# Kernel tuning notes

Hardware: AMD Instinct MI355X
Metric: run time of the kernel (lower is better)

Reference implementation:

```python
import jax, jax.numpy as jnp
import numpy as np

N_NODES = 50000
N_EDGES = 800000
D = 128


def gcn_conv(x, W, b, src, dst, num_nodes):
    """PyG GCNConv: x @ W, add self-loops, symmetric normalization, scatter-add, + bias."""
    x = x @ W  # [N, out]
    loop = jnp.arange(num_nodes, dtype=src.dtype)
    s = jnp.concatenate([src, loop])  # [E+N]
    d = jnp.concatenate([dst, loop])
    w = jnp.ones(s.shape[0], x.dtype)  # edge_weight=None -> ones (self-loop fill=1)
    deg = jax.ops.segment_sum(w, d, num_segments=num_nodes)  # [N]
    dinv = jnp.where(deg > 0, jax.lax.rsqrt(deg), 0.0)
    norm = dinv[s] * dinv[d]  # [E+N]
    out = jax.ops.segment_sum(x[s] * norm[:, None], d, num_segments=num_nodes)
    return out + b


def setup_inputs() -> dict:
    key = jax.random.key(0)
    ks = jax.random.split(key, 8)
    sc = 1.0 / np.sqrt(D)
    x = jax.random.normal(ks[0], (N_NODES, D), dtype=jnp.float32)
    edge_index = jax.random.randint(ks[1], (2, N_EDGES), 0, N_NODES)
    W1 = jax.random.normal(ks[2], (D, D), dtype=jnp.float32) * sc
    W2 = jax.random.normal(ks[3], (D, D), dtype=jnp.float32) * sc
    W3 = jax.random.normal(ks[4], (D, D), dtype=jnp.float32) * sc
    b1 = jnp.zeros((D,), jnp.float32)
    b2 = jnp.zeros((D,), jnp.float32)
    b3 = jnp.zeros((D,), jnp.float32)
    return {"x": x, "edge_index": edge_index, "W1": W1, "b1": b1,
            "W2": W2, "b2": b2, "W3": W3, "b3": b3}


def reference(x, edge_index, W1, b1, W2, b2, W3, b3):
    src, dst = edge_index[0], edge_index[1]
    n = x.shape[0]
    x = jax.nn.relu(gcn_conv(x, W1, b1, src, dst, n))
    x = jax.nn.relu(gcn_conv(x, W2, b2, src, dst, n))
    return gcn_conv(x, W3, b3, src, dst, n)
```

## Files before the change

### kernel.cpp

```cpp
#include <hip/hip_runtime.h>
#include <hip/hip_fp16.h>
#include <math.h>

#define D 128
#define PADH 136

typedef __attribute__((ext_vector_type(8))) _Float16 half8;
typedef __attribute__((ext_vector_type(4))) float f32x4;


__global__ void prep_kernel(const float* __restrict__ W1, const float* __restrict__ W2,
                            const float* __restrict__ W3, __half* __restrict__ WhT,
                            int* __restrict__ cnt, int N) {
    int i = blockIdx.x * blockDim.x + threadIdx.x;
    if (i < 3 * D * D) {
        int l = i >> 14;
        int j = i & 16383;
        int n = j >> 7, k = j & 127;
        const float* W = (l == 0) ? W1 : (l == 1) ? W2 : W3;
        WhT[(size_t)i] = __float2half(W[(size_t)k * D + n]);
    }
    if (i < N) cnt[i] = 0;
}


__global__ void count_rank_kernel(const int* __restrict__ dst, int* __restrict__ cnt,
                                  int* __restrict__ rank, int E) {
    int e0 = (blockIdx.x * blockDim.x + threadIdx.x) * 8;
    if (e0 + 7 < E) {
        int4 da = *(const int4*)(dst + e0);
        int4 db = *(const int4*)(dst + e0 + 4);
        int4 ra, rb;
        ra.x = atomicAdd(&cnt[da.x], 1);
        ra.y = atomicAdd(&cnt[da.y], 1);
        ra.z = atomicAdd(&cnt[da.z], 1);
        ra.w = atomicAdd(&cnt[da.w], 1);
        rb.x = atomicAdd(&cnt[db.x], 1);
        rb.y = atomicAdd(&cnt[db.y], 1);
        rb.z = atomicAdd(&cnt[db.z], 1);
        rb.w = atomicAdd(&cnt[db.w], 1);
        *(int4*)(rank + e0)     = ra;
        *(int4*)(rank + e0 + 4) = rb;
    } else {
        for (int e = e0; e < E; ++e) rank[e] = atomicAdd(&cnt[dst[e]], 1);
    }
}

__global__ __launch_bounds__(1024) void scan_kernel(const int* __restrict__ cnt,
                                                    int* __restrict__ rowptr,
                                                    float* __restrict__ dinv,
                                                    int N) {
    __shared__ int wsum[16];
    int tid  = threadIdx.x;
    int lane = tid & 63;
    int wid  = tid >> 6;
    int C = ((N + 4095) / 4096) * 4;
    int start = tid * C;
    int end   = start + C; if (end > N) end = N;

    int local = 0;
    int i = start;
    for (; i + 3 < end; i += 4) {
        int4 v = *(const int4*)(cnt + i);
        local += v.x + v.y + v.z + v.w;
    }
    for (; i < end; ++i) local += cnt[i];

    int sc = local;
    #pragma unroll
    for (int off = 1; off < 64; off <<= 1) {
        int t = __shfl_up(sc, off, 64);
        if (lane >= off) sc += t;
    }
    if (lane == 63) wsum[wid] = sc;
    __syncthreads();
    if (tid < 16) {
        int w = wsum[tid];
        #pragma unroll
        for (int off = 1; off < 16; off <<= 1) {
            int t = __shfl_up(w, off, 16);
            if (tid >= off) w += t;
        }
        wsum[tid] = w;
    }
    __syncthreads();
    int run = ((wid > 0) ? wsum[wid - 1] : 0) + (sc - local);

    i = start;
    for (; i + 3 < end; i += 4) {
        int4 v = *(const int4*)(cnt + i);
        int4 rp;
        rp.x = run;
        rp.y = rp.x + v.x;
        rp.z = rp.y + v.y;
        rp.w = rp.z + v.z;
        run  = rp.w + v.w;
        *(int4*)(rowptr + i) = rp;
        float4 dv;
        dv.x = rsqrtf((float)v.x + 1.0f);
        dv.y = rsqrtf((float)v.y + 1.0f);
        dv.z = rsqrtf((float)v.z + 1.0f);
        dv.w = rsqrtf((float)v.w + 1.0f);
        *(float4*)(dinv + i) = dv;
    }
    for (; i < end; ++i) {
        int v = cnt[i];
        rowptr[i] = run; run += v;
        dinv[i] = rsqrtf((float)v + 1.0f);
    }
    if (tid == 0) rowptr[N] = wsum[15];
}


#define GATHER(vv, cc) __half2 vv = ((const __half2*)(g + (size_t)(cc) * D))[lane]

__device__ __forceinline__ float2 gather_row(const __half* __restrict__ g,
                                             const int* __restrict__ rowptr,
                                             const int* __restrict__ col,
                                             int row, int lane) {
    int s = rowptr[row], e = rowptr[row + 1];
    __half2 hself = ((const __half2*)(g + (size_t)row * D))[lane];
    float2 a0 = __half22float2(hself);
    float2 a1 = make_float2(0.f, 0.f), a2 = make_float2(0.f, 0.f),
           a3 = make_float2(0.f, 0.f), a4 = make_float2(0.f, 0.f),
           a5 = make_float2(0.f, 0.f), a6 = make_float2(0.f, 0.f),
           a7 = make_float2(0.f, 0.f);

    for (int base = s; base < e; base += 64) {
        int idx = base + lane;
        int myc = (idx < e) ? col[idx] : 0;
        int nb  = min(64, e - base);
        int j = 0;
        for (; j + 16 <= nb; j += 16) {
            int c0 = __shfl(myc, j + 0),  c1 = __shfl(myc, j + 1);
            int c2 = __shfl(myc, j + 2),  c3 = __shfl(myc, j + 3);
            int c4 = __shfl(myc, j + 4),  c5 = __shfl(myc, j + 5);
            int c6 = __shfl(myc, j + 6),  c7 = __shfl(myc, j + 7);
            int c8 = __shfl(myc, j + 8),  c9 = __shfl(myc, j + 9);
            int cA = __shfl(myc, j + 10), cB = __shfl(myc, j + 11);
            int cC = __shfl(myc, j + 12), cD = __shfl(myc, j + 13);
            int cE = __shfl(myc, j + 14), cF = __shfl(myc, j + 15);
            GATHER(v0, c0); GATHER(v1, c1); GATHER(v2, c2); GATHER(v3, c3);
            GATHER(v4, c4); GATHER(v5, c5); GATHER(v6, c6); GATHER(v7, c7);
            GATHER(v8, c8); GATHER(v9, c9); GATHER(vA, cA); GATHER(vB, cB);
            GATHER(vC, cC); GATHER(vD, cD); GATHER(vE, cE); GATHER(vF, cF);
            a0.x += __low2float(v0); a0.y += __high2float(v0);
            a1.x += __low2float(v1); a1.y += __high2float(v1);
            a2.x += __low2float(v2); a2.y += __high2float(v2);
            a3.x += __low2float(v3); a3.y += __high2float(v3);
            a4.x += __low2float(v4); a4.y += __high2float(v4);
            a5.x += __low2float(v5); a5.y += __high2float(v5);
            a6.x += __low2float(v6); a6.y += __high2float(v6);
            a7.x += __low2float(v7); a7.y += __high2float(v7);
            a0.x += __low2float(v8); a0.y += __high2float(v8);
            a1.x += __low2float(v9); a1.y += __high2float(v9);
            a2.x += __low2float(vA); a2.y += __high2float(vA);
            a3.x += __low2float(vB); a3.y += __high2float(vB);
            a4.x += __low2float(vC); a4.y += __high2float(vC);
            a5.x += __low2float(vD); a5.y += __high2float(vD);
            a6.x += __low2float(vE); a6.y += __high2float(vE);
            a7.x += __low2float(vF); a7.y += __high2float(vF);
        }
        for (; j + 8 <= nb; j += 8) {
            int c0 = __shfl(myc, j + 0), c1 = __shfl(myc, j + 1);
            int c2 = __shfl(myc, j + 2), c3 = __shfl(myc, j + 3);
            int c4 = __shfl(myc, j + 4), c5 = __shfl(myc, j + 5);
            int c6 = __shfl(myc, j + 6), c7 = __shfl(myc, j + 7);
            GATHER(v0, c0); GATHER(v1, c1); GATHER(v2, c2); GATHER(v3, c3);
            GATHER(v4, c4); GATHER(v5, c5); GATHER(v6, c6); GATHER(v7, c7);
            a0.x += __low2float(v0); a0.y += __high2float(v0);
            a1.x += __low2float(v1); a1.y += __high2float(v1);
            a2.x += __low2float(v2); a2.y += __high2float(v2);
            a3.x += __low2float(v3); a3.y += __high2float(v3);
            a4.x += __low2float(v4); a4.y += __high2float(v4);
            a5.x += __low2float(v5); a5.y += __high2float(v5);
            a6.x += __low2float(v6); a6.y += __high2float(v6);
            a7.x += __low2float(v7); a7.y += __high2float(v7);
        }
        for (; j + 4 <= nb; j += 4) {
            int c0 = __shfl(myc, j + 0), c1 = __shfl(myc, j + 1);
            int c2 = __shfl(myc, j + 2), c3 = __shfl(myc, j + 3);
            GATHER(v0, c0); GATHER(v1, c1); GATHER(v2, c2); GATHER(v3, c3);
            a0.x += __low2float(v0); a0.y += __high2float(v0);
            a1.x += __low2float(v1); a1.y += __high2float(v1);
            a2.x += __low2float(v2); a2.y += __high2float(v2);
            a3.x += __low2float(v3); a3.y += __high2float(v3);
        }
        for (; j < nb; ++j) {
            int c = __shfl(myc, j);
            GATHER(v, c);
            a0.x += __low2float(v); a0.y += __high2float(v);
        }
    }
    a0.x += a1.x + a2.x + a3.x + a4.x + a5.x + a6.x + a7.x;
    a0.y += a1.y + a2.y + a3.y + a4.y + a5.y + a6.y + a7.y;
    return a0;
}


__global__ __launch_bounds__(256) void fill_gemm1_kernel(
    const int* __restrict__ src, const int* __restrict__ dst,
    const int* __restrict__ rank, const int* __restrict__ rowptr,
    int* __restrict__ col, int E, int fill_blocks,
    const float* __restrict__ X, const __half* __restrict__ WhT,
    const float* __restrict__ dinv, __half* __restrict__ Y, int M) {
    int tid = threadIdx.x;
    if ((int)blockIdx.x < fill_blocks) {
        int e0 = (blockIdx.x * 256 + tid) * 8;
        if (e0 + 7 < E) {
            int4 da = *(const int4*)(dst + e0);
            int4 db = *(const int4*)(dst + e0 + 4);
            int4 ra = *(const int4*)(rank + e0);
            int4 rb = *(const int4*)(rank + e0 + 4);
            int4 sa = *(const int4*)(src + e0);
            int4 sb = *(const int4*)(src + e0 + 4);
            int p0 = rowptr[da.x] + ra.x;
            int p1 = rowptr[da.y] + ra.y;
            int p2 = rowptr[da.z] + ra.z;
            int p3 = rowptr[da.w] + ra.w;
            int p4 = rowptr[db.x] + rb.x;
            int p5 = rowptr[db.y] + rb.y;
            int p6 = rowptr[db.z] + rb.z;
            int p7 = rowptr[db.w] + rb.w;
            col[p0] = sa.x; col[p1] = sa.y; col[p2] = sa.z; col[p3] = sa.w;
            col[p4] = sb.x; col[p5] = sb.y; col[p6] = sb.z; col[p7] = sb.w;
        } else {
            for (int e = e0; e < E; ++e) col[rowptr[dst[e]] + rank[e]] = src[e];
        }
        return;
    }
    int bid  = blockIdx.x - fill_blocks;
    int wave = tid >> 6;
    int lane = tid & 63;
    int quad = lane >> 4;
    int l16  = lane & 15;
    int m0   = bid * 64 + wave * 16;
    if (m0 >= M) return;

    f32x4 acc[8];
    #pragma unroll
    for (int t = 0; t < 8; ++t) acc[t] = (f32x4)0.0f;

    const float* xrow = X + (size_t)(m0 + l16) * D;

    #pragma unroll
    for (int ks = 0; ks < 4; ++ks) {
        int k0 = ks * 32 + quad * 8;
        float4 x0 = *(const float4*)(xrow + k0);
        float4 x1 = *(const float4*)(xrow + k0 + 4);
        half8 a;
        a[0] = (_Float16)x0.x; a[1] = (_Float16)x0.y;
        a[2] = (_Float16)x0.z; a[3] = (_Float16)x0.w;
        a[4] = (_Float16)x1.x; a[5] = (_Float16)x1.y;
        a[6] = (_Float16)x1.z; a[7] = (_Float16)x1.w;
        #pragma unroll
        for (int t = 0; t < 8; ++t) {
            half8 b = *(const half8*)(WhT + (size_t)(t * 16 + l16) * D + k0);
            acc[t] = __builtin_amdgcn_mfma_f32_16x16x32_f16(a, b, acc[t], 0, 0, 0);
        }
    }

    float4 dv = *(const float4*)(dinv + m0 + quad * 4);
    float dvs[4] = {dv.x, dv.y, dv.z, dv.w};
    #pragma unroll
    for (int t = 0; t < 8; ++t) {
        #pragma unroll
        for (int r = 0; r < 4; ++r) {
            int grow = m0 + quad * 4 + r;
            Y[(size_t)grow * D + t * 16 + l16] = __float2half(acc[t][r] * dvs[r]);
        }
    }
}


__global__ __launch_bounds__(256) void agg_gemm_kernel(
    const __half* __restrict__ ysIn, const int* __restrict__ rowptr,
    const int* __restrict__ col, const float* __restrict__ dinv,
    const float* __restrict__ bias, const __half* __restrict__ WhT,
    __half* __restrict__ ysOut, int M) {
    __shared__ __half lds_h[16 * PADH];
    int tid  = threadIdx.x;
    int wave = tid >> 6;
    int lane = tid & 63;
    int rbase = blockIdx.x * 16;

    float2 bb = ((const float2*)bias)[lane];
    #pragma unroll
    for (int t = 0; t < 4; ++t) {
        int row = rbase + wave * 4 + t;
        if (row < M) {
            float2 a = gather_row(ysIn, rowptr, col, row, lane);
            float dv = dinv[row];
            float rx = bb.x + dv * a.x;
            float ry = bb.y + dv * a.y;
            __half2 hv = __floats2half2_rn(fmaxf(rx, 0.f), fmaxf(ry, 0.f));
            ((__half2*)(lds_h + (size_t)(wave * 4 + t) * PADH))[lane] = hv;
        }
    }
    __syncthreads();

    if (rbase >= M) return;
    int quad = lane >> 4;
    int l16  = lane & 15;
    int t0   = wave * 2;

    f32x4 acc0 = (f32x4)0.0f, acc1 = (f32x4)0.0f;
    const __half* arow = lds_h + (size_t)l16 * PADH;

    #pragma unroll
    for (int ks = 0; ks < 4; ++ks) {
        int k0 = ks * 32 + quad * 8;
        half8 a  = *(const half8*)(arow + k0);
        half8 b0 = *(const half8*)(WhT + (size_t)((t0 + 0) * 16 + l16) * D + k0);
        half8 b1 = *(const half8*)(WhT + (size_t)((t0 + 1) * 16 + l16) * D + k0);
        acc0 = __builtin_amdgcn_mfma_f32_16x16x32_f16(a, b0, acc0, 0, 0, 0);
        acc1 = __builtin_amdgcn_mfma_f32_16x16x32_f16(a, b1, acc1, 0, 0, 0);
    }

    #pragma unroll
    for (int r = 0; r < 4; ++r) {
        int grow = rbase + quad * 4 + r;
        if (grow < M) {
            float dvr = dinv[grow];
            ysOut[(size_t)grow * D + (t0 + 0) * 16 + l16] = __float2half(acc0[r] * dvr);
            ysOut[(size_t)grow * D + (t0 + 1) * 16 + l16] = __float2half(acc1[r] * dvr);
        }
    }
}


__global__ __launch_bounds__(256) void agg_final_kernel(
    const __half* __restrict__ ys, const int* __restrict__ rowptr,
    const int* __restrict__ col, const float* __restrict__ dinv,
    const float* __restrict__ b, float* __restrict__ out, int N) {
    int gwave = (blockIdx.x * blockDim.x + threadIdx.x) >> 6;
    int lane  = threadIdx.x & 63;
    if (gwave >= N) return;
    float2 a  = gather_row(ys, rowptr, col, gwave, lane);
    float dv  = dinv[gwave];
    float2 bb = ((const float2*)b)[lane];
    ((float2*)(out + (size_t)gwave * D))[lane] = make_float2(bb.x + dv * a.x, bb.y + dv * a.y);
}


extern "C" void kernel_launch(void* const* d_in, const int* in_sizes, int n_in,
                              void* d_out, int out_size, void* d_ws, size_t ws_size,
                              hipStream_t stream) {
    const float* x   = (const float*)d_in[0];
    const int*   ei  = (const int*)d_in[1];
    const float* W1  = (const float*)d_in[2];
    const float* b1  = (const float*)d_in[3];
    const float* W2  = (const float*)d_in[4];
    const float* b2  = (const float*)d_in[5];
    const float* W3  = (const float*)d_in[6];
    const float* b3  = (const float*)d_in[7];
    float* out = (float*)d_out;

    const int N = in_sizes[0] / D;
    const int E = in_sizes[1] / 2;
    const int* src = ei;
    const int* dst = ei + E;

    char* ws = (char*)d_ws;
    size_t off = 0;
    auto alloc = [&](size_t bytes) {
        void* p = ws + off;
        off = (off + bytes + 255) & ~(size_t)255;
        return p;
    };
    __half* ys    = (__half*)alloc((size_t)N * D * sizeof(__half));
    __half* hs    = (__half*)alloc((size_t)N * D * sizeof(__half));
    int*   cnt    = (int*)alloc((size_t)N * sizeof(int));
    int*   rowptr = (int*)alloc((size_t)(N + 1) * sizeof(int));
    float* dinv   = (float*)alloc((size_t)N * sizeof(float));
    int*   rank   = (int*)alloc((size_t)E * sizeof(int));
    int*   col    = (int*)alloc((size_t)E * sizeof(int));
    __half* WhT   = (__half*)alloc((size_t)3 * D * D * sizeof(__half));
    (void)ws_size; (void)n_in; (void)out_size;

    int prep_threads = (3 * D * D > N) ? 3 * D * D : N;
    prep_kernel<<<(prep_threads + 255) / 256, 256, 0, stream>>>(W1, W2, W3, WhT, cnt, N);

    const int egrid = ((E + 7) / 8 + 255) / 256;
    count_rank_kernel<<<egrid, 256, 0, stream>>>(dst, cnt, rank, E);
    scan_kernel<<<1, 1024, 0, stream>>>(cnt, rowptr, dinv, N);

    const int gemm1_grid = (N + 63) / 64;
    fill_gemm1_kernel<<<egrid + gemm1_grid, 256, 0, stream>>>(
        src, dst, rank, rowptr, col, E, egrid, x, WhT, dinv, ys, N);

    const int agg_gemm_grid = (N + 15) / 16;
    agg_gemm_kernel<<<agg_gemm_grid, 256, 0, stream>>>(ys, rowptr, col, dinv, b1, WhT + 16384, hs, N);
    agg_gemm_kernel<<<agg_gemm_grid, 256, 0, stream>>>(hs, rowptr, col, dinv, b2, WhT + 32768, ys, N);

    const int agg_grid = (N * 64 + 255) / 256;
    agg_final_kernel<<<agg_grid, 256, 0, stream>>>(ys, rowptr, col, dinv, b3, out, N);
}
```

Before: 311.4 us.

## Build CSR with atomic cursors and use 8-wave blocks for agg_gemm

```diff
diff --git a/kernel.cpp b/kernel.cpp
--- a/kernel.cpp
+++ b/kernel.cpp
@@ -24,30 +24,27 @@
 }
 
 
-__global__ void count_rank_kernel(const int* __restrict__ dst, int* __restrict__ cnt,
-                                  int* __restrict__ rank, int E) {
+__global__ void count_kernel(const int* __restrict__ dst, int* __restrict__ cnt, int E) {
     int e0 = (blockIdx.x * blockDim.x + threadIdx.x) * 8;
     if (e0 + 7 < E) {
         int4 da = *(const int4*)(dst + e0);
         int4 db = *(const int4*)(dst + e0 + 4);
-        int4 ra, rb;
-        ra.x = atomicAdd(&cnt[da.x], 1);
-        ra.y = atomicAdd(&cnt[da.y], 1);
-        ra.z = atomicAdd(&cnt[da.z], 1);
-        ra.w = atomicAdd(&cnt[da.w], 1);
-        rb.x = atomicAdd(&cnt[db.x], 1);
-        rb.y = atomicAdd(&cnt[db.y], 1);
-        rb.z = atomicAdd(&cnt[db.z], 1);
-        rb.w = atomicAdd(&cnt[db.w], 1);
-        *(int4*)(rank + e0)     = ra;
-        *(int4*)(rank + e0 + 4) = rb;
+        atomicAdd(&cnt[da.x], 1);
+        atomicAdd(&cnt[da.y], 1);
+        atomicAdd(&cnt[da.z], 1);
+        atomicAdd(&cnt[da.w], 1);
+        atomicAdd(&cnt[db.x], 1);
+        atomicAdd(&cnt[db.y], 1);
+        atomicAdd(&cnt[db.z], 1);
+        atomicAdd(&cnt[db.w], 1);
     } else {
-        for (int e = e0; e < E; ++e) rank[e] = atomicAdd(&cnt[dst[e]], 1);
+        for (int e = e0; e < E; ++e) atomicAdd(&cnt[dst[e]], 1);
     }
 }
 
 __global__ __launch_bounds__(1024) void scan_kernel(const int* __restrict__ cnt,
                                                     int* __restrict__ rowptr,
+                                                    int* __restrict__ cursor,
                                                     float* __restrict__ dinv,
                                                     int N) {
     __shared__ int wsum[16];
@@ -96,6 +93,7 @@
         rp.w = rp.z + v.z;
         run  = rp.w + v.w;
         *(int4*)(rowptr + i) = rp;
+        *(int4*)(cursor + i) = rp;
         float4 dv;
         dv.x = rsqrtf((float)v.x + 1.0f);
         dv.y = rsqrtf((float)v.y + 1.0f);
@@ -105,7 +103,7 @@
     }
     for (; i < end; ++i) {
         int v = cnt[i];
-        rowptr[i] = run; run += v;
+        rowptr[i] = run; cursor[i] = run; run += v;
         dinv[i] = rsqrtf((float)v + 1.0f);
     }
     if (tid == 0) rowptr[N] = wsum[15];
@@ -200,8 +198,7 @@
 
 __global__ __launch_bounds__(256) void fill_gemm1_kernel(
     const int* __restrict__ src, const int* __restrict__ dst,
-    const int* __restrict__ rank, const int* __restrict__ rowptr,
-    int* __restrict__ col, int E, int fill_blocks,
+    int* __restrict__ cursor, int* __restrict__ col, int E, int fill_blocks,
     const float* __restrict__ X, const __half* __restrict__ WhT,
     const float* __restrict__ dinv, __half* __restrict__ Y, int M) {
     int tid = threadIdx.x;
@@ -210,22 +207,23 @@
         if (e0 + 7 < E) {
             int4 da = *(const int4*)(dst + e0);
             int4 db = *(const int4*)(dst + e0 + 4);
-            int4 ra = *(const int4*)(rank + e0);
-            int4 rb = *(const int4*)(rank + e0 + 4);
             int4 sa = *(const int4*)(src + e0);
             int4 sb = *(const int4*)(src + e0 + 4);
-            int p0 = rowptr[da.x] + ra.x;
-            int p1 = rowptr[da.y] + ra.y;
-            int p2 = rowptr[da.z] + ra.z;
-            int p3 = rowptr[da.w] + ra.w;
-            int p4 = rowptr[db.x] + rb.x;
-            int p5 = rowptr[db.y] + rb.y;
-            int p6 = rowptr[db.z] + rb.z;
-            int p7 = rowptr[db.w] + rb.w;
+            int p0 = atomicAdd(&cursor[da.x], 1);
+            int p1 = atomicAdd(&cursor[da.y], 1);
+            int p2 = atomicAdd(&cursor[da.z], 1);
+            int p3 = atomicAdd(&cursor[da.w], 1);
+            int p4 = atomicAdd(&cursor[db.x], 1);
+            int p5 = atomicAdd(&cursor[db.y], 1);
+            int p6 = atomicAdd(&cursor[db.z], 1);
+            int p7 = atomicAdd(&cursor[db.w], 1);
             col[p0] = sa.x; col[p1] = sa.y; col[p2] = sa.z; col[p3] = sa.w;
             col[p4] = sb.x; col[p5] = sb.y; col[p6] = sb.z; col[p7] = sb.w;
         } else {
-            for (int e = e0; e < E; ++e) col[rowptr[dst[e]] + rank[e]] = src[e];
+            for (int e = e0; e < E; ++e) {
+                int p = atomicAdd(&cursor[dst[e]], 1);
+                col[p] = src[e];
+            }
         }
         return;
     }
@@ -273,7 +271,7 @@
 }
 
 
-__global__ __launch_bounds__(256) void agg_gemm_kernel(
+__global__ __launch_bounds__(512) void agg_gemm_kernel(
     const __half* __restrict__ ysIn, const int* __restrict__ rowptr,
     const int* __restrict__ col, const float* __restrict__ dinv,
     const float* __restrict__ bias, const __half* __restrict__ WhT,
@@ -286,15 +284,16 @@
 
     float2 bb = ((const float2*)bias)[lane];
     #pragma unroll
-    for (int t = 0; t < 4; ++t) {
-        int row = rbase + wave * 4 + t;
+    for (int t = 0; t < 2; ++t) {
+        int r   = wave * 2 + t;
+        int row = rbase + r;
         if (row < M) {
             float2 a = gather_row(ysIn, rowptr, col, row, lane);
             float dv = dinv[row];
             float rx = bb.x + dv * a.x;
             float ry = bb.y + dv * a.y;
             __half2 hv = __floats2half2_rn(fmaxf(rx, 0.f), fmaxf(ry, 0.f));
-            ((__half2*)(lds_h + (size_t)(wave * 4 + t) * PADH))[lane] = hv;
+            ((__half2*)(lds_h + (size_t)r * PADH))[lane] = hv;
         }
     }
     __syncthreads();
@@ -302,19 +301,16 @@
     if (rbase >= M) return;
     int quad = lane >> 4;
     int l16  = lane & 15;
-    int t0   = wave * 2;
-
-    f32x4 acc0 = (f32x4)0.0f, acc1 = (f32x4)0.0f;
+
+    f32x4 acc = (f32x4)0.0f;
     const __half* arow = lds_h + (size_t)l16 * PADH;
 
     #pragma unroll
     for (int ks = 0; ks < 4; ++ks) {
         int k0 = ks * 32 + quad * 8;
-        half8 a  = *(const half8*)(arow + k0);
-        half8 b0 = *(const half8*)(WhT + (size_t)((t0 + 0) * 16 + l16) * D + k0);
-        half8 b1 = *(const half8*)(WhT + (size_t)((t0 + 1) * 16 + l16) * D + k0);
-        acc0 = __builtin_amdgcn_mfma_f32_16x16x32_f16(a, b0, acc0, 0, 0, 0);
-        acc1 = __builtin_amdgcn_mfma_f32_16x16x32_f16(a, b1, acc1, 0, 0, 0);
+        half8 a = *(const half8*)(arow + k0);
+        half8 b = *(const half8*)(WhT + (size_t)(wave * 16 + l16) * D + k0);
+        acc = __builtin_amdgcn_mfma_f32_16x16x32_f16(a, b, acc, 0, 0, 0);
     }
 
     #pragma unroll
@@ -322,8 +318,7 @@
         int grow = rbase + quad * 4 + r;
         if (grow < M) {
             float dvr = dinv[grow];
-            ysOut[(size_t)grow * D + (t0 + 0) * 16 + l16] = __float2half(acc0[r] * dvr);
-            ysOut[(size_t)grow * D + (t0 + 1) * 16 + l16] = __float2half(acc1[r] * dvr);
+            ysOut[(size_t)grow * D + wave * 16 + l16] = __float2half(acc[r] * dvr);
         }
     }
 }
@@ -372,8 +367,8 @@
     __half* hs    = (__half*)alloc((size_t)N * D * sizeof(__half));
     int*   cnt    = (int*)alloc((size_t)N * sizeof(int));
     int*   rowptr = (int*)alloc((size_t)(N + 1) * sizeof(int));
+    int*   cursor = (int*)alloc((size_t)N * sizeof(int));
     float* dinv   = (float*)alloc((size_t)N * sizeof(float));
-    int*   rank   = (int*)alloc((size_t)E * sizeof(int));
     int*   col    = (int*)alloc((size_t)E * sizeof(int));
     __half* WhT   = (__half*)alloc((size_t)3 * D * D * sizeof(__half));
     (void)ws_size; (void)n_in; (void)out_size;
@@ -382,16 +377,16 @@
     prep_kernel<<<(prep_threads + 255) / 256, 256, 0, stream>>>(W1, W2, W3, WhT, cnt, N);
 
     const int egrid = ((E + 7) / 8 + 255) / 256;
-    count_rank_kernel<<<egrid, 256, 0, stream>>>(dst, cnt, rank, E);
-    scan_kernel<<<1, 1024, 0, stream>>>(cnt, rowptr, dinv, N);
+    count_kernel<<<egrid, 256, 0, stream>>>(dst, cnt, E);
+    scan_kernel<<<1, 1024, 0, stream>>>(cnt, rowptr, cursor, dinv, N);
 
     const int gemm1_grid = (N + 63) / 64;
     fill_gemm1_kernel<<<egrid + gemm1_grid, 256, 0, stream>>>(
-        src, dst, rank, rowptr, col, E, egrid, x, WhT, dinv, ys, N);
+        src, dst, cursor, col, E, egrid, x, WhT, dinv, ys, N);
 
     const int agg_gemm_grid = (N + 15) / 16;
-    agg_gemm_kernel<<<agg_gemm_grid, 256, 0, stream>>>(ys, rowptr, col, dinv, b1, WhT + 16384, hs, N);
-    agg_gemm_kernel<<<agg_gemm_grid, 256, 0, stream>>>(hs, rowptr, col, dinv, b2, WhT + 32768, ys, N);
+    agg_gemm_kernel<<<agg_gemm_grid, 512, 0, stream>>>(ys, rowptr, col, dinv, b1, WhT + 16384, hs, N);
+    agg_gemm_kernel<<<agg_gemm_grid, 512, 0, stream>>>(hs, rowptr, col, dinv, b2, WhT + 32768, ys, N);
 
     const int agg_grid = (N * 64 + 255) / 256;
     agg_final_kernel<<<agg_grid, 256, 0, stream>>>(ys, rowptr, col, dinv, b3, out, N);
```

After: 340.5 us. +9.3%, slower.

## Split each wave into two half-waves gathering separate rows with 8-byte loads

Applied to the files above, without the earlier changes.

```diff
diff --git a/kernel.cpp b/kernel.cpp
--- a/kernel.cpp
+++ b/kernel.cpp
@@ -6,6 +6,7 @@
 #define PADH 136
 
 typedef __attribute__((ext_vector_type(8))) _Float16 half8;
+typedef __attribute__((ext_vector_type(4))) _Float16 half4v;
 typedef __attribute__((ext_vector_type(4))) float f32x4;
 
 
@@ -112,89 +113,67 @@
 }
 
 
-#define GATHER(vv, cc) __half2 vv = ((const __half2*)(g + (size_t)(cc) * D))[lane]
-
-__device__ __forceinline__ float2 gather_row(const __half* __restrict__ g,
-                                             const int* __restrict__ rowptr,
-                                             const int* __restrict__ col,
-                                             int row, int lane) {
+__device__ __forceinline__ float4 gather2(const __half* __restrict__ g,
+                                          const int* __restrict__ rowptr,
+                                          const int* __restrict__ col,
+                                          int r0, int r1, int lane) {
+    int half = lane >> 5;
+    int l32  = lane & 31;
+    int hb   = half << 5;
+    int row  = half ? r1 : r0;
     int s = rowptr[row], e = rowptr[row + 1];
-    __half2 hself = ((const __half2*)(g + (size_t)row * D))[lane];
-    float2 a0 = __half22float2(hself);
-    float2 a1 = make_float2(0.f, 0.f), a2 = make_float2(0.f, 0.f),
-           a3 = make_float2(0.f, 0.f), a4 = make_float2(0.f, 0.f),
-           a5 = make_float2(0.f, 0.f), a6 = make_float2(0.f, 0.f),
-           a7 = make_float2(0.f, 0.f);
-
-    for (int base = s; base < e; base += 64) {
-        int idx = base + lane;
+
+    half4v hs = ((const half4v*)(g + (size_t)row * D))[l32];
+    float4 A = make_float4((float)hs[0], (float)hs[1], (float)hs[2], (float)hs[3]);
+    float4 B = make_float4(0.f, 0.f, 0.f, 0.f);
+
+    for (int base = s; base < e; base += 32) {
+        int idx = base + l32;
         int myc = (idx < e) ? col[idx] : 0;
-        int nb  = min(64, e - base);
+        int nb  = min(32, e - base);
         int j = 0;
-        for (; j + 16 <= nb; j += 16) {
-            int c0 = __shfl(myc, j + 0),  c1 = __shfl(myc, j + 1);
-            int c2 = __shfl(myc, j + 2),  c3 = __shfl(myc, j + 3);
-            int c4 = __shfl(myc, j + 4),  c5 = __shfl(myc, j + 5);
-            int c6 = __shfl(myc, j + 6),  c7 = __shfl(myc, j + 7);
-            int c8 = __shfl(myc, j + 8),  c9 = __shfl(myc, j + 9);
-            int cA = __shfl(myc, j + 10), cB = __shfl(myc, j + 11);
-            int cC = __shfl(myc, j + 12), cD = __shfl(myc, j + 13);
-            int cE = __shfl(myc, j + 14), cF = __shfl(myc, j + 15);
-            GATHER(v0, c0); GATHER(v1, c1); GATHER(v2, c2); GATHER(v3, c3);
-            GATHER(v4, c4); GATHER(v5, c5); GATHER(v6, c6); GATHER(v7, c7);
-            GATHER(v8, c8); GATHER(v9, c9); GATHER(vA, cA); GATHER(vB, cB);
-            GATHER(vC, cC); GATHER(vD, cD); GATHER(vE, cE); GATHER(vF, cF);
-            a0.x += __low2float(v0); a0.y += __high2float(v0);
-            a1.x += __low2float(v1); a1.y += __high2float(v1);
-            a2.x += __low2float(v2); a2.y += __high2float(v2);
-            a3.x += __low2float(v3); a3.y += __high2float(v3);
-            a4.x += __low2float(v4); a4.y += __high2float(v4);
-            a5.x += __low2float(v5); a5.y += __high2float(v5);
-            a6.x += __low2float(v6); a6.y += __high2float(v6);
-            a7.x += __low2float(v7); a7.y += __high2float(v7);
-            a0.x += __low2float(v8); a0.y += __high2float(v8);
-            a1.x += __low2float(v9); a1.y += __high2float(v9);
-            a2.x += __low2float(vA); a2.y += __high2float(vA);
-            a3.x += __low2float(vB); a3.y += __high2float(vB);
-            a4.x += __low2float(vC); a4.y += __high2float(vC);
-            a5.x += __low2float(vD); a5.y += __high2float(vD);
-            a6.x += __low2float(vE); a6.y += __high2float(vE);
-            a7.x += __low2float(vF); a7.y += __high2float(vF);
-        }
         for (; j + 8 <= nb; j += 8) {
-            int c0 = __shfl(myc, j + 0), c1 = __shfl(myc, j + 1);
-            int c2 = __shfl(myc, j + 2), c3 = __shfl(myc, j + 3);
-            int c4 = __shfl(myc, j + 4), c5 = __shfl(myc, j + 5);
-            int c6 = __shfl(myc, j + 6), c7 = __shfl(myc, j + 7);
-            GATHER(v0, c0); GATHER(v1, c1); GATHER(v2, c2); GATHER(v3, c3);
-            GATHER(v4, c4); GATHER(v5, c5); GATHER(v6, c6); GATHER(v7, c7);
-            a0.x += __low2float(v0); a0.y += __high2float(v0);
-            a1.x += __low2float(v1); a1.y += __high2float(v1);
-            a2.x += __low2float(v2); a2.y += __high2float(v2);
-            a3.x += __low2float(v3); a3.y += __high2float(v3);
-            a4.x += __low2float(v4); a4.y += __high2float(v4);
-            a5.x += __low2float(v5); a5.y += __high2float(v5);
-            a6.x += __low2float(v6); a6.y += __high2float(v6);
-            a7.x += __low2float(v7); a7.y += __high2float(v7);
+            int c0 = __shfl(myc, hb + j + 0), c1 = __shfl(myc, hb + j + 1);
+            int c2 = __shfl(myc, hb + j + 2), c3 = __shfl(myc, hb + j + 3);
+            int c4 = __shfl(myc, hb + j + 4), c5 = __shfl(myc, hb + j + 5);
+            int c6 = __shfl(myc, hb + j + 6), c7 = __shfl(myc, hb + j + 7);
+            half4v v0 = ((const half4v*)(g + (size_t)c0 * D))[l32];
+            half4v v1 = ((const half4v*)(g + (size_t)c1 * D))[l32];
+            half4v v2 = ((const half4v*)(g + (size_t)c2 * D))[l32];
+            half4v v3 = ((const half4v*)(g + (size_t)c3 * D))[l32];
+            half4v v4 = ((const half4v*)(g + (size_t)c4 * D))[l32];
+            half4v v5 = ((const half4v*)(g + (size_t)c5 * D))[l32];
+            half4v v6 = ((const half4v*)(g + (size_t)c6 * D))[l32];
+            half4v v7 = ((const half4v*)(g + (size_t)c7 * D))[l32];
+            A.x += (float)v0[0]; A.y += (float)v0[1]; A.z += (float)v0[2]; A.w += (float)v0[3];
+            B.x += (float)v1[0]; B.y += (float)v1[1]; B.z += (float)v1[2]; B.w += (float)v1[3];
+            A.x += (float)v2[0]; A.y += (float)v2[1]; A.z += (float)v2[2]; A.w += (float)v2[3];
+            B.x += (float)v3[0]; B.y += (float)v3[1]; B.z += (float)v3[2]; B.w += (float)v3[3];
+            A.x += (float)v4[0]; A.y += (float)v4[1]; A.z += (float)v4[2]; A.w += (float)v4[3];
+            B.x += (float)v5[0]; B.y += (float)v5[1]; B.z += (float)v5[2]; B.w += (float)v5[3];
+            A.x += (float)v6[0]; A.y += (float)v6[1]; A.z += (float)v6[2]; A.w += (float)v6[3];
+            B.x += (float)v7[0]; B.y += (float)v7[1]; B.z += (float)v7[2]; B.w += (float)v7[3];
         }
         for (; j + 4 <= nb; j += 4) {
-            int c0 = __shfl(myc, j + 0), c1 = __shfl(myc, j + 1);
-            int c2 = __shfl(myc, j + 2), c3 = __shfl(myc, j + 3);
-            GATHER(v0, c0); GATHER(v1, c1); GATHER(v2, c2); GATHER(v3, c3);
-            a0.x += __low2float(v0); a0.y += __high2float(v0);
-            a1.x += __low2float(v1); a1.y += __high2float(v1);
-            a2.x += __low2float(v2); a2.y += __high2float(v2);
-            a3.x += __low2float(v3); a3.y += __high2float(v3);
+            int c0 = __shfl(myc, hb + j + 0), c1 = __shfl(myc, hb + j + 1);
+            int c2 = __shfl(myc, hb + j + 2), c3 = __shfl(myc, hb + j + 3);
+            half4v v0 = ((const half4v*)(g + (size_t)c0 * D))[l32];
+            half4v v1 = ((const half4v*)(g + (size_t)c1 * D))[l32];
+            half4v v2 = ((const half4v*)(g + (size_t)c2 * D))[l32];
+            half4v v3 = ((const half4v*)(g + (size_t)c3 * D))[l32];
+            A.x += (float)v0[0]; A.y += (float)v0[1]; A.z += (float)v0[2]; A.w += (float)v0[3];
+            B.x += (float)v1[0]; B.y += (float)v1[1]; B.z += (float)v1[2]; B.w += (float)v1[3];
+            A.x += (float)v2[0]; A.y += (float)v2[1]; A.z += (float)v2[2]; A.w += (float)v2[3];
+            B.x += (float)v3[0]; B.y += (float)v3[1]; B.z += (float)v3[2]; B.w += (float)v3[3];
         }
         for (; j < nb; ++j) {
-            int c = __shfl(myc, j);
-            GATHER(v, c);
-            a0.x += __low2float(v); a0.y += __high2float(v);
-        }
-    }
-    a0.x += a1.x + a2.x + a3.x + a4.x + a5.x + a6.x + a7.x;
-    a0.y += a1.y + a2.y + a3.y + a4.y + a5.y + a6.y + a7.y;
-    return a0;
+            int c = __shfl(myc, hb + j);
+            half4v v = ((const half4v*)(g + (size_t)c * D))[l32];
+            A.x += (float)v[0]; A.y += (float)v[1]; A.z += (float)v[2]; A.w += (float)v[3];
+        }
+    }
+    A.x += B.x; A.y += B.y; A.z += B.z; A.w += B.w;
+    return A;
 }
 
 
@@ -282,20 +261,27 @@
     int tid  = threadIdx.x;
     int wave = tid >> 6;
     int lane = tid & 63;
+    int half = lane >> 5;
+    int l32  = lane & 31;
     int rbase = blockIdx.x * 16;
 
-    float2 bb = ((const float2*)bias)[lane];
-    #pragma unroll
-    for (int t = 0; t < 4; ++t) {
-        int row = rbase + wave * 4 + t;
-        if (row < M) {
-            float2 a = gather_row(ysIn, rowptr, col, row, lane);
-            float dv = dinv[row];
-            float rx = bb.x + dv * a.x;
-            float ry = bb.y + dv * a.y;
-            __half2 hv = __floats2half2_rn(fmaxf(rx, 0.f), fmaxf(ry, 0.f));
-            ((__half2*)(lds_h + (size_t)(wave * 4 + t) * PADH))[lane] = hv;
-        }
+    float4 bb = ((const float4*)bias)[l32];
+    #pragma unroll
+    for (int t = 0; t < 2; ++t) {
+        int lr0 = wave * 4 + t * 2;
+        int row0 = rbase + lr0;
+        int row1 = row0 + 1;
+        int c0 = min(row0, M - 1);
+        int c1 = min(row1, M - 1);
+        float4 a = gather2(ysIn, rowptr, col, c0, c1, lane);
+        int myrow = half ? c1 : c0;
+        float dv = dinv[myrow];
+        half4v hv;
+        hv[0] = (_Float16)fmaxf(bb.x + dv * a.x, 0.f);
+        hv[1] = (_Float16)fmaxf(bb.y + dv * a.y, 0.f);
+        hv[2] = (_Float16)fmaxf(bb.z + dv * a.z, 0.f);
+        hv[3] = (_Float16)fmaxf(bb.w + dv * a.w, 0.f);
+        ((half4v*)(lds_h + (size_t)(lr0 + half) * PADH))[l32] = hv;
     }
     __syncthreads();
 
@@ -335,11 +321,26 @@
     const float* __restrict__ b, float* __restrict__ out, int N) {
     int gwave = (blockIdx.x * blockDim.x + threadIdx.x) >> 6;
     int lane  = threadIdx.x & 63;
-    if (gwave >= N) return;
-    float2 a  = gather_row(ys, rowptr, col, gwave, lane);
-    float dv  = dinv[gwave];
-    float2 bb = ((const float2*)b)[lane];
-    ((float2*)(out + (size_t)gwave * D))[lane] = make_float2(bb.x + dv * a.x, bb.y + dv * a.y);
+    int half  = lane >> 5;
+    int l32   = lane & 31;
+    int row0  = gwave * 2;
+    if (row0 >= N) return;
+    int row1  = row0 + 1;
+    int c1    = min(row1, N - 1);
+
+    float4 a = gather2(ys, rowptr, col, row0, c1, lane);
+    int myrow = half ? c1 : row0;
+    int orow  = row0 + half;
+    if (orow < N) {
+        float dv  = dinv[myrow];
+        float4 bb = ((const float4*)b)[l32];
+        float4 r;
+        r.x = bb.x + dv * a.x;
+        r.y = bb.y + dv * a.y;
+        r.z = bb.z + dv * a.z;
+        r.w = bb.w + dv * a.w;
+        ((float4*)(out + (size_t)orow * D))[l32] = r;
+    }
 }
 
 
@@ -393,6 +394,6 @@
     agg_gemm_kernel<<<agg_gemm_grid, 256, 0, stream>>>(ys, rowptr, col, dinv, b1, WhT + 16384, hs, N);
     agg_gemm_kernel<<<agg_gemm_grid, 256, 0, stream>>>(hs, rowptr, col, dinv, b2, WhT + 32768, ys, N);
 
-    const int agg_grid = (N * 64 + 255) / 256;
-    agg_final_kernel<<<agg_grid, 256, 0, stream>>>(ys, rowptr, col, dinv, b3, out, N);
-}
+    const int aggf_grid = ((N + 1) / 2 * 64 + 255) / 256;
+    agg_final_kernel<<<aggf_grid, 256, 0, stream>>>(ys, rowptr, col, dinv, b3, out, N);
+}
```

Result: faster. 294.2 us (-5.5%).

## Slice features into 16-wide column blocks so gathers stay cache-resident

Applied to the files above, without the earlier changes.

```diff
diff --git a/kernel.cpp b/kernel.cpp
--- a/kernel.cpp
+++ b/kernel.cpp
@@ -3,10 +3,10 @@
 #include <math.h>
 
 #define D 128
-#define PADH 136
 
 typedef __attribute__((ext_vector_type(8))) _Float16 half8;
 typedef __attribute__((ext_vector_type(4))) float f32x4;
+
 
 
 __global__ void prep_kernel(const float* __restrict__ W1, const float* __restrict__ W2,
@@ -109,92 +109,6 @@
         dinv[i] = rsqrtf((float)v + 1.0f);
     }
     if (tid == 0) rowptr[N] = wsum[15];
-}
-
-
-#define GATHER(vv, cc) __half2 vv = ((const __half2*)(g + (size_t)(cc) * D))[lane]
-
-__device__ __forceinline__ float2 gather_row(const __half* __restrict__ g,
-                                             const int* __restrict__ rowptr,
-                                             const int* __restrict__ col,
-                                             int row, int lane) {
-    int s = rowptr[row], e = rowptr[row + 1];
-    __half2 hself = ((const __half2*)(g + (size_t)row * D))[lane];
-    float2 a0 = __half22float2(hself);
-    float2 a1 = make_float2(0.f, 0.f), a2 = make_float2(0.f, 0.f),
-           a3 = make_float2(0.f, 0.f), a4 = make_float2(0.f, 0.f),
-           a5 = make_float2(0.f, 0.f), a6 = make_float2(0.f, 0.f),
-           a7 = make_float2(0.f, 0.f);
-
-    for (int base = s; base < e; base += 64) {
-        int idx = base + lane;
-        int myc = (idx < e) ? col[idx] : 0;
-        int nb  = min(64, e - base);
-        int j = 0;
-        for (; j + 16 <= nb; j += 16) {
-            int c0 = __shfl(myc, j + 0),  c1 = __shfl(myc, j + 1);
-            int c2 = __shfl(myc, j + 2),  c3 = __shfl(myc, j + 3);
-            int c4 = __shfl(myc, j + 4),  c5 = __shfl(myc, j + 5);
-            int c6 = __shfl(myc, j + 6),  c7 = __shfl(myc, j + 7);
-            int c8 = __shfl(myc, j + 8),  c9 = __shfl(myc, j + 9);
-            int cA = __shfl(myc, j + 10), cB = __shfl(myc, j + 11);
-            int cC = __shfl(myc, j + 12), cD = __shfl(myc, j + 13);
-            int cE = __shfl(myc, j + 14), cF = __shfl(myc, j + 15);
-            GATHER(v0, c0); GATHER(v1, c1); GATHER(v2, c2); GATHER(v3, c3);
-            GATHER(v4, c4); GATHER(v5, c5); GATHER(v6, c6); GATHER(v7, c7);
-            GATHER(v8, c8); GATHER(v9, c9); GATHER(vA, cA); GATHER(vB, cB);
-            GATHER(vC, cC); GATHER(vD, cD); GATHER(vE, cE); GATHER(vF, cF);
-            a0.x += __low2float(v0); a0.y += __high2float(v0);
-            a1.x += __low2float(v1); a1.y += __high2float(v1);
-            a2.x += __low2float(v2); a2.y += __high2float(v2);
-            a3.x += __low2float(v3); a3.y += __high2float(v3);
-            a4.x += __low2float(v4); a4.y += __high2float(v4);
-            a5.x += __low2float(v5); a5.y += __high2float(v5);
-            a6.x += __low2float(v6); a6.y += __high2float(v6);
-            a7.x += __low2float(v7); a7.y += __high2float(v7);
-            a0.x += __low2float(v8); a0.y += __high2float(v8);
-            a1.x += __low2float(v9); a1.y += __high2float(v9);
-            a2.x += __low2float(vA); a2.y += __high2float(vA);
-            a3.x += __low2float(vB); a3.y += __high2float(vB);
-            a4.x += __low2float(vC); a4.y += __high2float(vC);
-            a5.x += __low2float(vD); a5.y += __high2float(vD);
-            a6.x += __low2float(vE); a6.y += __high2float(vE);
-            a7.x += __low2float(vF); a7.y += __high2float(vF);
-        }
-        for (; j + 8 <= nb; j += 8) {
-            int c0 = __shfl(myc, j + 0), c1 = __shfl(myc, j + 1);
-            int c2 = __shfl(myc, j + 2), c3 = __shfl(myc, j + 3);
-            int c4 = __shfl(myc, j + 4), c5 = __shfl(myc, j + 5);
-            int c6 = __shfl(myc, j + 6), c7 = __shfl(myc, j + 7);
-            GATHER(v0, c0); GATHER(v1, c1); GATHER(v2, c2); GATHER(v3, c3);
-            GATHER(v4, c4); GATHER(v5, c5); GATHER(v6, c6); GATHER(v7, c7);
-            a0.x += __low2float(v0); a0.y += __high2float(v0);
-            a1.x += __low2float(v1); a1.y += __high2float(v1);
-            a2.x += __low2float(v2); a2.y += __high2float(v2);
-            a3.x += __low2float(v3); a3.y += __high2float(v3);
-            a4.x += __low2float(v4); a4.y += __high2float(v4);
-            a5.x += __low2float(v5); a5.y += __high2float(v5);
-            a6.x += __low2float(v6); a6.y += __high2float(v6);
-            a7.x += __low2float(v7); a7.y += __high2float(v7);
-        }
-        for (; j + 4 <= nb; j += 4) {
-            int c0 = __shfl(myc, j + 0), c1 = __shfl(myc, j + 1);
-            int c2 = __shfl(myc, j + 2), c3 = __shfl(myc, j + 3);
-            GATHER(v0, c0); GATHER(v1, c1); GATHER(v2, c2); GATHER(v3, c3);
-            a0.x += __low2float(v0); a0.y += __high2float(v0);
-            a1.x += __low2float(v1); a1.y += __high2float(v1);
-            a2.x += __low2float(v2); a2.y += __high2float(v2);
-            a3.x += __low2float(v3); a3.y += __high2float(v3);
-        }
-        for (; j < nb; ++j) {
-            int c = __shfl(myc, j);
-            GATHER(v, c);
-            a0.x += __low2float(v); a0.y += __high2float(v);
-        }
-    }
-    a0.x += a1.x + a2.x + a3.x + a4.x + a5.x + a6.x + a7.x;
-    a0.y += a1.y + a2.y + a3.y + a4.y + a5.y + a6.y + a7.y;
-    return a0;
 }
 
 
@@ -267,79 +181,132 @@
         #pragma unroll
         for (int r = 0; r < 4; ++r) {
             int grow = m0 + quad * 4 + r;
-            Y[(size_t)grow * D + t * 16 + l16] = __float2half(acc[t][r] * dvs[r]);
-        }
-    }
-}
-
-
-__global__ __launch_bounds__(256) void agg_gemm_kernel(
-    const __half* __restrict__ ysIn, const int* __restrict__ rowptr,
-    const int* __restrict__ col, const float* __restrict__ dinv,
-    const float* __restrict__ bias, const __half* __restrict__ WhT,
-    __half* __restrict__ ysOut, int M) {
-    __shared__ __half lds_h[16 * PADH];
+            Y[((size_t)t * M + grow) * 16 + l16] = __float2half(acc[t][r] * dvs[r]);
+        }
+    }
+}
+
+
+__global__ __launch_bounds__(256) void gemm_s_kernel(const __half* __restrict__ Xs,
+                                                     const __half* __restrict__ WhT,
+                                                     const float* __restrict__ dinv,
+                                                     __half* __restrict__ Ys, int M) {
     int tid  = threadIdx.x;
     int wave = tid >> 6;
     int lane = tid & 63;
-    int rbase = blockIdx.x * 16;
-
-    float2 bb = ((const float2*)bias)[lane];
-    #pragma unroll
-    for (int t = 0; t < 4; ++t) {
-        int row = rbase + wave * 4 + t;
-        if (row < M) {
-            float2 a = gather_row(ysIn, rowptr, col, row, lane);
-            float dv = dinv[row];
-            float rx = bb.x + dv * a.x;
-            float ry = bb.y + dv * a.y;
-            __half2 hv = __floats2half2_rn(fmaxf(rx, 0.f), fmaxf(ry, 0.f));
-            ((__half2*)(lds_h + (size_t)(wave * 4 + t) * PADH))[lane] = hv;
-        }
-    }
-    __syncthreads();
-
-    if (rbase >= M) return;
     int quad = lane >> 4;
     int l16  = lane & 15;
-    int t0   = wave * 2;
-
-    f32x4 acc0 = (f32x4)0.0f, acc1 = (f32x4)0.0f;
-    const __half* arow = lds_h + (size_t)l16 * PADH;
+    int m0   = blockIdx.x * 64 + wave * 16;
+    if (m0 >= M) return;
+
+    f32x4 acc[8];
+    #pragma unroll
+    for (int t = 0; t < 8; ++t) acc[t] = (f32x4)0.0f;
+
+    int arow = m0 + l16;
 
     #pragma unroll
     for (int ks = 0; ks < 4; ++ks) {
         int k0 = ks * 32 + quad * 8;
-        half8 a  = *(const half8*)(arow + k0);
-        half8 b0 = *(const half8*)(WhT + (size_t)((t0 + 0) * 16 + l16) * D + k0);
-        half8 b1 = *(const half8*)(WhT + (size_t)((t0 + 1) * 16 + l16) * D + k0);
-        acc0 = __builtin_amdgcn_mfma_f32_16x16x32_f16(a, b0, acc0, 0, 0, 0);
-        acc1 = __builtin_amdgcn_mfma_f32_16x16x32_f16(a, b1, acc1, 0, 0, 0);
-    }
-
-    #pragma unroll
-    for (int r = 0; r < 4; ++r) {
-        int grow = rbase + quad * 4 + r;
-        if (grow < M) {
-            float dvr = dinv[grow];
-            ysOut[(size_t)grow * D + (t0 + 0) * 16 + l16] = __float2half(acc0[r] * dvr);
-            ysOut[(size_t)grow * D + (t0 + 1) * 16 + l16] = __float2half(acc1[r] * dvr);
-        }
-    }
-}
-
-
-__global__ __launch_bounds__(256) void agg_final_kernel(
-    const __half* __restrict__ ys, const int* __restrict__ rowptr,
+        half8 a = *(const half8*)(Xs + ((size_t)(k0 >> 4) * M + arow) * 16 + (k0 & 15));
+        #pragma unroll
+        for (int t = 0; t < 8; ++t) {
+            half8 b = *(const half8*)(WhT + (size_t)(t * 16 + l16) * D + k0);
+            acc[t] = __builtin_amdgcn_mfma_f32_16x16x32_f16(a, b, acc[t], 0, 0, 0);
+        }
+    }
+
+    float4 dv = *(const float4*)(dinv + m0 + quad * 4);
+    float dvs[4] = {dv.x, dv.y, dv.z, dv.w};
+    #pragma unroll
+    for (int t = 0; t < 8; ++t) {
+        #pragma unroll
+        for (int r = 0; r < 4; ++r) {
+            int grow = m0 + quad * 4 + r;
+            Ys[((size_t)t * M + grow) * 16 + l16] = __float2half(acc[t][r] * dvs[r]);
+        }
+    }
+}
+
+
+template <bool FINAL>
+__global__ __launch_bounds__(256) void agg_slice_kernel(
+    const __half* __restrict__ ysIn, const int* __restrict__ rowptr,
     const int* __restrict__ col, const float* __restrict__ dinv,
-    const float* __restrict__ b, float* __restrict__ out, int N) {
-    int gwave = (blockIdx.x * blockDim.x + threadIdx.x) >> 6;
-    int lane  = threadIdx.x & 63;
-    if (gwave >= N) return;
-    float2 a  = gather_row(ys, rowptr, col, gwave, lane);
-    float dv  = dinv[gwave];
-    float2 bb = ((const float2*)b)[lane];
-    ((float2*)(out + (size_t)gwave * D))[lane] = make_float2(bb.x + dv * a.x, bb.y + dv * a.y);
+    const float* __restrict__ bias, __half* __restrict__ outh,
+    float* __restrict__ outf, int M) {
+    int bid   = blockIdx.x;
+    int slice = bid & 7;
+    int chunk = bid >> 3;
+    int tid  = threadIdx.x;
+    int wave = tid >> 6;
+    int lane = tid & 63;
+    int g    = lane >> 3;
+    int l8   = lane & 7;
+    int row  = chunk * 32 + wave * 8 + g;
+    bool valid = row < M;
+    int c = valid ? row : M - 1;
+
+    const __half* base = ysIn + (size_t)slice * M * 16;
+    int s = rowptr[c], e = rowptr[c + 1];
+
+    float2 bb = ((const float2*)bias)[slice * 8 + l8];
+
+    __half2 hself = *(const __half2*)(base + (size_t)c * 16 + l8 * 2);
+    float a0x = __low2float(hself), a0y = __high2float(hself);
+    float a1x = 0.f, a1y = 0.f, a2x = 0.f, a2y = 0.f, a3x = 0.f, a3y = 0.f;
+
+    int j = s;
+    for (; j + 8 <= e; j += 8) {
+        int c0 = col[j + 0], c1 = col[j + 1], c2 = col[j + 2], c3 = col[j + 3];
+        int c4 = col[j + 4], c5 = col[j + 5], c6 = col[j + 6], c7 = col[j + 7];
+        __half2 v0 = *(const __half2*)(base + (size_t)c0 * 16 + l8 * 2);
+        __half2 v1 = *(const __half2*)(base + (size_t)c1 * 16 + l8 * 2);
+        __half2 v2 = *(const __half2*)(base + (size_t)c2 * 16 + l8 * 2);
+        __half2 v3 = *(const __half2*)(base + (size_t)c3 * 16 + l8 * 2);
+        __half2 v4 = *(const __half2*)(base + (size_t)c4 * 16 + l8 * 2);
+        __half2 v5 = *(const __half2*)(base + (size_t)c5 * 16 + l8 * 2);
+        __half2 v6 = *(const __half2*)(base + (size_t)c6 * 16 + l8 * 2);
+        __half2 v7 = *(const __half2*)(base + (size_t)c7 * 16 + l8 * 2);
+        a0x += __low2float(v0); a0y += __high2float(v0);
+        a1x += __low2float(v1); a1y += __high2float(v1);
+        a2x += __low2float(v2); a2y += __high2float(v2);
+        a3x += __low2float(v3); a3y += __high2float(v3);
+        a0x += __low2float(v4); a0y += __high2float(v4);
+        a1x += __low2float(v5); a1y += __high2float(v5);
+        a2x += __low2float(v6); a2y += __high2float(v6);
+        a3x += __low2float(v7); a3y += __high2float(v7);
+    }
+    for (; j + 4 <= e; j += 4) {
+        int c0 = col[j + 0], c1 = col[j + 1], c2 = col[j + 2], c3 = col[j + 3];
+        __half2 v0 = *(const __half2*)(base + (size_t)c0 * 16 + l8 * 2);
+        __half2 v1 = *(const __half2*)(base + (size_t)c1 * 16 + l8 * 2);
+        __half2 v2 = *(const __half2*)(base + (size_t)c2 * 16 + l8 * 2);
+        __half2 v3 = *(const __half2*)(base + (size_t)c3 * 16 + l8 * 2);
+        a0x += __low2float(v0); a0y += __high2float(v0);
+        a1x += __low2float(v1); a1y += __high2float(v1);
+        a2x += __low2float(v2); a2y += __high2float(v2);
+        a3x += __low2float(v3); a3y += __high2float(v3);
+    }
+    for (; j < e; ++j) {
+        int c0 = col[j];
+        __half2 v0 = *(const __half2*)(base + (size_t)c0 * 16 + l8 * 2);
+        a0x += __low2float(v0); a0y += __high2float(v0);
+    }
+    a0x += a1x + a2x + a3x;
+    a0y += a1y + a2y + a3y;
+
+    float dv = dinv[c];
+    float rx = bb.x + dv * a0x;
+    float ry = bb.y + dv * a0y;
+    if (valid) {
+        if (FINAL) {
+            *(float2*)(outf + (size_t)row * D + slice * 16 + l8 * 2) = make_float2(rx, ry);
+        } else {
+            __half2 hv = __floats2half2_rn(fmaxf(rx, 0.f), fmaxf(ry, 0.f));
+            *(__half2*)(outh + ((size_t)slice * M + row) * 16 + l8 * 2) = hv;
+        }
+    }
 }
 
 
@@ -385,14 +352,15 @@
     count_rank_kernel<<<egrid, 256, 0, stream>>>(dst, cnt, rank, E);
     scan_kernel<<<1, 1024, 0, stream>>>(cnt, rowptr, dinv, N);
 
-    const int gemm1_grid = (N + 63) / 64;
-    fill_gemm1_kernel<<<egrid + gemm1_grid, 256, 0, stream>>>(
+    const int gemm_grid = (N + 63) / 64;
+    fill_gemm1_kernel<<<egrid + gemm_grid, 256, 0, stream>>>(
         src, dst, rank, rowptr, col, E, egrid, x, WhT, dinv, ys, N);
 
-    const int agg_gemm_grid = (N + 15) / 16;
-    agg_gemm_kernel<<<agg_gemm_grid, 256, 0, stream>>>(ys, rowptr, col, dinv, b1, WhT + 16384, hs, N);
-    agg_gemm_kernel<<<agg_gemm_grid, 256, 0, stream>>>(hs, rowptr, col, dinv, b2, WhT + 32768, ys, N);
-
-    const int agg_grid = (N * 64 + 255) / 256;
-    agg_final_kernel<<<agg_grid, 256, 0, stream>>>(ys, rowptr, col, dinv, b3, out, N);
-}
+    const int nchunk = (N + 31) / 32;
+    const int agg_grid = nchunk * 8;
+    agg_slice_kernel<false><<<agg_grid, 256, 0, stream>>>(ys, rowptr, col, dinv, b1, hs, nullptr, N);
+    gemm_s_kernel<<<gemm_grid, 256, 0, stream>>>(hs, WhT + 16384, dinv, ys, N);
+    agg_slice_kernel<false><<<agg_grid, 256, 0, stream>>>(ys, rowptr, col, dinv, b2, hs, nullptr, N);
+    gemm_s_kernel<<<gemm_grid, 256, 0, stream>>>(hs, WhT + 32768, dinv, ys, N);
+    agg_slice_kernel<true><<<agg_grid, 256, 0, stream>>>(ys, rowptr, col, dinv, b3, nullptr, out, N);
+}
```

Result: slower. 345.2 us (+10.8%).
